# Kernel optimization log

Hardware: AMD Instinct MI355X
Metric: run time of the kernel (lower is better)

The kernel has to match this reference:

```python
import jax, jax.numpy as jnp
import numpy as np

N_NODES = 100000
N_EDGES = 6400000

def setup_inputs() -> dict:
    key = jax.random.key(0)
    ks = jax.random.split(key, 12)
    x = jax.random.normal(ks[0], (N_NODES, 2), dtype=jnp.float32)
    edge_index = jax.random.randint(ks[1], (2, N_EDGES), 0, N_NODES, dtype=jnp.int32)
    def w(k, fi, fo):
        return jax.random.normal(k, (fi, fo), dtype=jnp.float32) * (1.0 / np.sqrt(fi))
    return {
        "x": x, "edge_index": edge_index,
        "W0": w(ks[2], 2, 8), "b0": jnp.zeros((8,), jnp.float32),
        "W1": w(ks[3], 8, 8), "b1": jnp.zeros((8,), jnp.float32),
        "W2": w(ks[4], 8, 8), "b2": jnp.zeros((8,), jnp.float32),
        "W3": w(ks[5], 8, 8), "b3": jnp.zeros((8,), jnp.float32),
        "Wv": w(ks[6], 8, 1), "bv": jnp.zeros((1,), jnp.float32),
        "Wp": w(ks[7], 8, 1), "bp": jnp.zeros((1,), jnp.float32),
    }

def _gcn_norm(edge_index, n_nodes):
    # PyG GCNConv default: add self-loops, symmetric D^{-1/2} A_hat D^{-1/2}
    loops = jnp.arange(n_nodes, dtype=edge_index.dtype)
    src = jnp.concatenate([edge_index[0], loops])
    dst = jnp.concatenate([edge_index[1], loops])
    deg = jax.ops.segment_sum(jnp.ones_like(dst, dtype=jnp.float32), dst,
                              num_segments=n_nodes)
    dis = jax.lax.rsqrt(jnp.maximum(deg, 1.0))  # deg >= 1 due to self-loops
    norm = dis[src] * dis[dst]                   # [E + N]
    return src, dst, norm

def _gcn_conv(x, W, b, src, dst, norm, n_nodes):
    h = x @ W                                     # small GEMM [N, fo]
    msg = h[src] * norm[:, None]                  # gather + normalize
    out = jax.ops.segment_sum(msg, dst, num_segments=n_nodes)  # scatter-add
    return out + b

def reference(x, edge_index, W0, b0, W1, b1, W2, b2, W3, b3, Wv, bv, Wp, bp):
    n = x.shape[0]
    src, dst, norm = _gcn_norm(edge_index, n)
    h = x
    for W, b in ((W0, b0), (W1, b1), (W2, b2), (W3, b3)):
        h = jax.nn.elu(_gcn_conv(h, W, b, src, dst, norm, n))
    mean_val = _gcn_conv(h, Wv, bv, src, dst, norm, n)   # [N, 1]
    value = jnp.mean(mean_val, axis=0, keepdims=True)    # global_mean_pool, 1 graph -> [1, 1]
    proba = _gcn_conv(h, Wp, bp, src, dst, norm, n)      # [N, 1]
    return (proba, value)
```

## Files before the change

### kernel.cpp

```cpp
#include <hip/hip_runtime.h>

#define NT 256
#define CHUNK 1024
#define PBLK2 2048
#define PTILE 4096

static inline int nbi(long long n) { return (int)((n + NT - 1) / NT); }


__global__ __launch_bounds__(256) void k_histB(const int* __restrict__ dst,
                                               int* __restrict__ histB,
                                               int E, int NB) {
    __shared__ int lh[512];
    int t = threadIdx.x;
    for (int i = t; i < 512; i += 256) lh[i] = 0;
    __syncthreads();
    int chunk = (E + gridDim.x - 1) / gridDim.x;
    int lo = blockIdx.x * chunk, hi = min(E, lo + chunk);
    for (int i = lo + t; i < hi; i += 256)
        atomicAdd(&lh[dst[i] >> 8], 1);
    __syncthreads();
    for (int b = t; b < NB; b += 256)
        histB[(size_t)blockIdx.x * NB + b] = lh[b];
}

__global__ __launch_bounds__(256) void k_scanB2(const int* __restrict__ histB,
                                                int* __restrict__ cursorT,
                                                int* __restrict__ tot,
                                                int NB, int nblk) {
    __shared__ int ch[256];
    __shared__ int carry;
    int b = blockIdx.x, t = threadIdx.x;
    if (t == 0) carry = 0;
    __syncthreads();
    for (int c = 0; c < nblk; c += 256) {
        int blk = c + t;
        int v = (blk < nblk) ? histB[(size_t)blk * NB + b] : 0;
        ch[t] = v;
        __syncthreads();
        for (int o = 1; o < 256; o <<= 1) {
            int x = (t >= o) ? ch[t - o] : 0;
            __syncthreads();
            ch[t] += x;
            __syncthreads();
        }
        int excl = ch[t] - v + carry;
        if (blk < nblk) cursorT[(size_t)b * PBLK2 + blk] = excl;
        __syncthreads();
        if (t == 0) carry += ch[255];
        __syncthreads();
    }
    if (t == 0) tot[b] = carry;
}

__global__ __launch_bounds__(512) void k_bscan(const int* __restrict__ hist_g,
                                               int* __restrict__ bbase,
                                               int* __restrict__ rowst,
                                               int NB, int N, int E) {
    __shared__ int s[512];
    int t = threadIdx.x;
    int own = (t < NB) ? hist_g[t] : 0;
    s[t] = own;
    __syncthreads();
    for (int o = 1; o < 512; o <<= 1) {
        int v = (t >= o) ? s[t - o] : 0;
        __syncthreads();
        s[t] += v;
        __syncthreads();
    }
    if (t < NB) bbase[t] = s[t] - own;
    if (t == 0) { bbase[NB] = E; rowst[N] = E; }
}

__global__ __launch_bounds__(256) void k_partF(const int* __restrict__ src,
                                               const int* __restrict__ dst,
                                               const int* __restrict__ bbase,
                                               const int* __restrict__ cursorT,
                                               int* __restrict__ part,
                                               int E, int NB) {
    __shared__ int wcur[512];
    __shared__ int th[512], tloff[512], tcnt[512];
    __shared__ int ps[256];
    __shared__ int stage[PTILE];
    __shared__ unsigned short sbkt[PTILE];
    int t = threadIdx.x;
    int chunk = (E + gridDim.x - 1) / gridDim.x;
    int lo = blockIdx.x * chunk, hi = min(E, lo + chunk);
    if (lo >= hi) return;

    for (int b = t; b < NB; b += 256)
        wcur[b] = bbase[b] + cursorT[(size_t)b * PBLK2 + blockIdx.x];
    __syncthreads();

    for (int tlo = lo; tlo < hi; tlo += PTILE) {
        int thi = min(hi, tlo + PTILE);
        int cnt = thi - tlo;
        for (int i = t; i < 512; i += 256) { th[i] = 0; tcnt[i] = 0; }
        __syncthreads();
        for (int i = tlo + t; i < thi; i += 256) atomicAdd(&th[dst[i] >> 8], 1);
        __syncthreads();
        int a0 = th[2 * t], a1 = th[2 * t + 1];
        int psum = a0 + a1;
        ps[t] = psum;
        __syncthreads();
        for (int o = 1; o < 256; o <<= 1) {
            int v = (t >= o) ? ps[t - o] : 0;
            __syncthreads();
            ps[t] += v;
            __syncthreads();
        }
        int excl = ps[t] - psum;
        tloff[2 * t] = excl;
        tloff[2 * t + 1] = excl + a0;
        __syncthreads();
        for (int i = tlo + t; i < thi; i += 256) {
            int d = dst[i], s = src[i];
            int b = d >> 8;
            int pos = tloff[b] + atomicAdd(&tcnt[b], 1);
            stage[pos] = ((d & 255) << 17) | s;
            sbkt[pos] = (unsigned short)b;
        }
        __syncthreads();
        for (int i = t; i < cnt; i += 256) {
            int b = sbkt[i];
            part[wcur[b] + (i - tloff[b])] = stage[i];
        }
        __syncthreads();
        for (int b = t; b < NB; b += 256) wcur[b] += th[b];
        __syncthreads();
    }
}

__global__ __launch_bounds__(512) void k_build(const int* __restrict__ bbase,
                                               const int* __restrict__ part,
                                               const float* __restrict__ x,
                                               int* __restrict__ rowst,
                                               float* __restrict__ dis,
                                               float* __restrict__ v0,
                                               int* __restrict__ csr,
                                               int N) {
    __shared__ int dcnt[256], doff[256];
    int b = blockIdx.x, t = threadIdx.x;
    int lo = bbase[b], hi = bbase[b + 1];
    if (t < 256) dcnt[t] = 0;
    __syncthreads();
    for (int i = lo + t; i < hi; i += 512)
        atomicAdd(&dcnt[part[i] >> 17], 1);
    __syncthreads();
    int own = 0;
    if (t < 256) { own = dcnt[t]; doff[t] = own; }
    __syncthreads();
    for (int o = 1; o < 256; o <<= 1) {
        int v = 0;
        if (t < 256 && t >= o) v = doff[t - o];
        __syncthreads();
        if (t < 256) doff[t] += v;
        __syncthreads();
    }
    if (t < 256) {
        int excl = doff[t] - own;
        int node = (b << 8) + t;
        if (node < N) {
            rowst[node] = lo + excl;
            float dn = rsqrtf((float)own + 1.0f);
            dis[node] = dn;
            float2 xv = *reinterpret_cast<const float2*>(x + 2 * node);
            *reinterpret_cast<float2*>(v0 + 2 * node) = make_float2(dn * xv.x, dn * xv.y);
        }
        dcnt[t] = excl;
    }
    __syncthreads();
    for (int i = lo + t; i < hi; i += 512) {
        int pv = part[i];
        int slot = atomicAdd(&dcnt[pv >> 17], 1);
        csr[lo + slot] = pv & 0x1FFFF;
    }
}


__global__ __launch_bounds__(NT) void k_gL1(const int* __restrict__ rowst,
                                            const int* __restrict__ csr,
                                            const float* __restrict__ dis,
                                            const float* __restrict__ v0,
                                            const float* __restrict__ W0,
                                            const float* __restrict__ b0,
                                            const float* __restrict__ W1,
                                            float* __restrict__ un, int N) {
    int g = blockIdx.x * NT + threadIdx.x;
    int n = g >> 3, sub = g & 7;
    if (n >= N) return;
    int i = rowst[n] + sub, end = rowst[n + 1];
    float ax = 0.0f, ay = 0.0f;
    int s0 = 0, s1 = 0;
    bool r0 = i < end, r1 = i + 8 < end;
    if (r0) s0 = csr[i];
    if (r1) s1 = csr[i + 8];
    while (r0) {
        float2 p = *reinterpret_cast<const float2*>(v0 + 2 * s0);
        int i2 = i + 16;
        bool r2 = i2 < end;
        int s2 = 0; if (r2) s2 = csr[i2];
        ax += p.x; ay += p.y;
        i += 8; r0 = r1; s0 = s1; r1 = r2; s1 = s2;
    }
    ax += __shfl_xor(ax, 1, 64); ax += __shfl_xor(ax, 2, 64); ax += __shfl_xor(ax, 4, 64);
    ay += __shfl_xor(ay, 1, 64); ay += __shfl_xor(ay, 2, 64); ay += __shfl_xor(ay, 4, 64);
    float2 sv = *reinterpret_cast<const float2*>(v0 + 2 * n);
    ax += sv.x; ay += sv.y;
    float dn = dis[n];
    float gg = dn * (ax * W0[sub] + ay * W0[8 + sub]) + b0[sub];
    float h = gg > 0.0f ? gg : expm1f(gg);
    int base = (threadIdx.x & 63) & ~7;
    float o = 0.0f;
#pragma unroll
    for (int k = 0; k < 8; ++k) o += __shfl(h, base + k, 64) * W1[k * 8 + sub];
    un[8 * n + sub] = dn * o;
}

__global__ __launch_bounds__(NT) void k_gL8(const int* __restrict__ rowst,
                                            const int* __restrict__ csr,
                                            const float* __restrict__ dis,
                                            const float* __restrict__ u,
                                            const float* __restrict__ b,
                                            const float* __restrict__ W,
                                            float* __restrict__ un, int N) {
    int g = blockIdx.x * NT + threadIdx.x;
    int n = g >> 3, sub = g & 7;
    if (n >= N) return;
    int i = rowst[n] + sub, end = rowst[n + 1];
    float a[8];
#pragma unroll
    for (int k = 0; k < 8; ++k) a[k] = 0.0f;
    int s0 = 0, s1 = 0;
    bool r0 = i < end, r1 = i + 8 < end;
    if (r0) s0 = csr[i];
    if (r1) s1 = csr[i + 8];
    while (r0) {
        float4 p0 = *reinterpret_cast<const float4*>(u + 8 * s0);
        float4 p1 = *reinterpret_cast<const float4*>(u + 8 * s0 + 4);
        int i2 = i + 16;
        bool r2 = i2 < end;
        int s2 = 0; if (r2) s2 = csr[i2];
        a[0] += p0.x; a[1] += p0.y; a[2] += p0.z; a[3] += p0.w;
        a[4] += p1.x; a[5] += p1.y; a[6] += p1.z; a[7] += p1.w;
        i += 8; r0 = r1; s0 = s1; r1 = r2; s1 = s2;
    }
    int c4 = sub & 4, c2 = sub & 2, c1 = sub & 1;
#pragma unroll
    for (int j = 0; j < 4; ++j) {
        float send = c4 ? a[j] : a[j + 4];
        float recv = __shfl_xor(send, 4, 64);
        a[j] = (c4 ? a[j + 4] : a[j]) + recv;
    }
#pragma unroll
    for (int j = 0; j < 2; ++j) {
        float send = c2 ? a[j] : a[j + 2];
        float recv = __shfl_xor(send, 2, 64);
        a[j] = (c2 ? a[j + 2] : a[j]) + recv;
    }
    {
        float send = c1 ? a[0] : a[1];
        float recv = __shfl_xor(send, 1, 64);
        a[0] = (c1 ? a[1] : a[0]) + recv;
    }
    float dn = dis[n];
    float va = a[0] + u[8 * n + sub];
    float gg = va * dn + b[sub];
    float h = gg > 0.0f ? gg : expm1f(gg);
    int base = (threadIdx.x & 63) & ~7;
    float o = 0.0f;
#pragma unroll
    for (int k = 0; k < 8; ++k) o += __shfl(h, base + k, 64) * W[k * 8 + sub];
    un[8 * n + sub] = dn * o;
}

__global__ __launch_bounds__(NT) void k_gHead(const int* __restrict__ rowst,
                                              const int* __restrict__ csr,
                                              const float* __restrict__ dis,
                                              const float* __restrict__ u,
                                              const float* __restrict__ b,
                                              const float* __restrict__ Wv,
                                              const float* __restrict__ Wp,
                                              float* __restrict__ uH, int N) {
    int g = blockIdx.x * NT + threadIdx.x;
    int n = g >> 3, sub = g & 7;
    if (n >= N) return;
    int i = rowst[n] + sub, end = rowst[n + 1];
    float a[8];
#pragma unroll
    for (int k = 0; k < 8; ++k) a[k] = 0.0f;
    int s0 = 0, s1 = 0;
    bool r0 = i < end, r1 = i + 8 < end;
    if (r0) s0 = csr[i];
    if (r1) s1 = csr[i + 8];
    while (r0) {
        float4 p0 = *reinterpret_cast<const float4*>(u + 8 * s0);
        float4 p1 = *reinterpret_cast<const float4*>(u + 8 * s0 + 4);
        int i2 = i + 16;
        bool r2 = i2 < end;
        int s2 = 0; if (r2) s2 = csr[i2];
        a[0] += p0.x; a[1] += p0.y; a[2] += p0.z; a[3] += p0.w;
        a[4] += p1.x; a[5] += p1.y; a[6] += p1.z; a[7] += p1.w;
        i += 8; r0 = r1; s0 = s1; r1 = r2; s1 = s2;
    }
    int c4 = sub & 4, c2 = sub & 2, c1 = sub & 1;
#pragma unroll
    for (int j = 0; j < 4; ++j) {
        float send = c4 ? a[j] : a[j + 4];
        float recv = __shfl_xor(send, 4, 64);
        a[j] = (c4 ? a[j + 4] : a[j]) + recv;
    }
#pragma unroll
    for (int j = 0; j < 2; ++j) {
        float send = c2 ? a[j] : a[j + 2];
        float recv = __shfl_xor(send, 2, 64);
        a[j] = (c2 ? a[j + 2] : a[j]) + recv;
    }
    {
        float send = c1 ? a[0] : a[1];
        float recv = __shfl_xor(send, 1, 64);
        a[0] = (c1 ? a[1] : a[0]) + recv;
    }
    float dn = dis[n];
    float va = a[0] + u[8 * n + sub];
    float gg = va * dn + b[sub];
    float h = gg > 0.0f ? gg : expm1f(gg);
    float tv = h * Wv[sub];
    float tp = h * Wp[sub];
    tv += __shfl_xor(tv, 1, 64); tv += __shfl_xor(tv, 2, 64); tv += __shfl_xor(tv, 4, 64);
    tp += __shfl_xor(tp, 1, 64); tp += __shfl_xor(tp, 2, 64); tp += __shfl_xor(tp, 4, 64);
    if (sub == 0)
        *reinterpret_cast<float2*>(uH + 2 * n) = make_float2(dn * tv, dn * tp);
}

__global__ __launch_bounds__(NT) void k_g2F(const int* __restrict__ rowst,
                                            const int* __restrict__ csr,
                                            const float* __restrict__ dis,
                                            const float* __restrict__ uH,
                                            const float* __restrict__ bp,
                                            float* __restrict__ out,
                                            float* __restrict__ vsum, int N) {
    int g = blockIdx.x * NT + threadIdx.x;
    int n = g >> 3, sub = g & 7;
    bool valid = n < N;
    int i = 0, end = 0;
    if (valid) { i = rowst[n] + sub; end = rowst[n + 1]; }
    float av = 0.0f, ap = 0.0f;
    int s0 = 0, s1 = 0;
    bool r0 = i < end, r1 = i + 8 < end;
    if (r0) s0 = csr[i];
    if (r1) s1 = csr[i + 8];
    while (r0) {
        float2 p = *reinterpret_cast<const float2*>(uH + 2 * s0);
        int i2 = i + 16;
        bool r2 = i2 < end;
        int s2 = 0; if (r2) s2 = csr[i2];
        av += p.x; ap += p.y;
        i = i + 8; r0 = r1; s0 = s1; r1 = r2; s1 = s2;
    }
    av += __shfl_xor(av, 1, 64); av += __shfl_xor(av, 2, 64); av += __shfl_xor(av, 4, 64);
    ap += __shfl_xor(ap, 1, 64); ap += __shfl_xor(ap, 2, 64); ap += __shfl_xor(ap, 4, 64);
    float contrib = 0.0f;
    if (valid && sub == 0) {
        float2 selfv = *reinterpret_cast<const float2*>(uH + 2 * n);
        av += selfv.x; ap += selfv.y;
        float dn = dis[n];
        out[n] = ap * dn + bp[0];
        contrib = av * dn;
    }
#pragma unroll
    for (int o = 32; o > 0; o >>= 1) contrib += __shfl_down(contrib, o, 64);
    __shared__ float sred[NT / 64];
    if ((threadIdx.x & 63) == 0) sred[threadIdx.x >> 6] = contrib;
    __syncthreads();
    if (threadIdx.x == 0) {
        float bsum = 0.0f;
#pragma unroll
        for (int k = 0; k < NT / 64; ++k) bsum += sred[k];
        atomicAdd(vsum, bsum);
    }
}

__global__ void k_final(const float* __restrict__ vsum,
                        const float* __restrict__ bv,
                        float* __restrict__ out, int N) {
    out[0] = vsum[0] * (1.0f / (float)N) + bv[0];
}


__global__ __launch_bounds__(NT) void k_count(const int* __restrict__ dst,
                                              int* __restrict__ deg, int E) {
    int e = blockIdx.x * NT + threadIdx.x;
    if (e < E) atomicAdd(&deg[dst[e]], 1);
}

__global__ __launch_bounds__(NT) void k_scanA(const int* __restrict__ deg,
                                              int* __restrict__ partial, int N) {
    int t = threadIdx.x;
    int base = blockIdx.x * CHUNK + t * 4;
    int s = 0;
#pragma unroll
    for (int j = 0; j < 4; ++j) { int i = base + j; if (i < N) s += deg[i]; }
    __shared__ int red[NT];
    red[t] = s; __syncthreads();
    for (int o = NT / 2; o > 0; o >>= 1) {
        if (t < o) red[t] += red[t + o];
        __syncthreads();
    }
    if (t == 0) partial[blockIdx.x] = red[0];
}

__global__ void k_scanB(const int* __restrict__ partial, int* __restrict__ chunkoff,
                        int* __restrict__ rowst, int nblk, int N) {
    if (threadIdx.x == 0) {
        int off = 0;
        for (int b = 0; b < nblk; ++b) { chunkoff[b] = off; off += partial[b]; }
        rowst[N] = off;
    }
}

__global__ __launch_bounds__(NT) void k_scanC(const int* __restrict__ deg,
                                              const int* __restrict__ chunkoff,
                                              int* __restrict__ rowst,
                                              float* __restrict__ dis, int N) {
    int t = threadIdx.x;
    int base = blockIdx.x * CHUNK + t * 4;
    int v[4]; int tsum = 0;
#pragma unroll
    for (int j = 0; j < 4; ++j) { int i = base + j; v[j] = (i < N) ? deg[i] : 0; tsum += v[j]; }
    __shared__ int ss[NT];
    ss[t] = tsum; __syncthreads();
    for (int o = 1; o < NT; o <<= 1) {
        int x = (t >= o) ? ss[t - o] : 0;
        __syncthreads();
        ss[t] += x;
        __syncthreads();
    }
    int run = ss[t] - tsum + chunkoff[blockIdx.x];
#pragma unroll
    for (int j = 0; j < 4; ++j) {
        int i = base + j;
        if (i < N) { rowst[i] = run; dis[i] = rsqrtf((float)v[j] + 1.0f); run += v[j]; }
    }
}

__global__ __launch_bounds__(NT) void k_fill(const int* __restrict__ src,
                                             const int* __restrict__ dst,
                                             const int* __restrict__ rowst,
                                             int* __restrict__ deg,
                                             int* __restrict__ csr, int E) {
    int e = blockIdx.x * NT + threadIdx.x;
    if (e >= E) return;
    int s = src[e], d = dst[e];
    int old = atomicSub(&deg[d], 1);
    csr[rowst[d] + old - 1] = s;
}

__global__ __launch_bounds__(NT) void k_v0(const float* __restrict__ x,
                                           const float* __restrict__ dis,
                                           float* __restrict__ v0, int N) {
    int n = blockIdx.x * NT + threadIdx.x;
    if (n >= N) return;
    float dn = dis[n];
    float2 xv = *reinterpret_cast<const float2*>(x + 2 * n);
    *reinterpret_cast<float2*>(v0 + 2 * n) = make_float2(dn * xv.x, dn * xv.y);
}


extern "C" void kernel_launch(void* const* d_in, const int* in_sizes, int n_in,
                              void* d_out, int out_size, void* d_ws, size_t ws_size,
                              hipStream_t stream) {
    const float* x  = (const float*)d_in[0];
    const int* ei   = (const int*)d_in[1];
    const float* W0 = (const float*)d_in[2];
    const float* b0 = (const float*)d_in[3];
    const float* W1 = (const float*)d_in[4];
    const float* b1 = (const float*)d_in[5];
    const float* W2 = (const float*)d_in[6];
    const float* b2 = (const float*)d_in[7];
    const float* W3 = (const float*)d_in[8];
    const float* b3 = (const float*)d_in[9];
    const float* Wv = (const float*)d_in[10];
    const float* bv = (const float*)d_in[11];
    const float* Wp = (const float*)d_in[12];
    const float* bp = (const float*)d_in[13];
    float* out = (float*)d_out;

    int N = in_sizes[0] / 2;
    int E = in_sizes[1] / 2;
    const int* src = ei;
    const int* dst = ei + E;
    int NB = (N + 255) >> 8;

    size_t needP = ((size_t)22 * N + 2 * (size_t)E + 2048) * 4;
    bool histFits = (size_t)2 * PBLK2 * NB <= (size_t)E;

    if (N <= 131072 && NB <= 512 && ws_size >= needP && histFits) {
        int* tot    = (int*)d_ws;
        int* bbase  = tot + 512;
        float* vsum = (float*)(bbase + 513);
        int* rowst  = (int*)(vsum + 8);
        float* dis  = (float*)(rowst + N + 1);
        float* v0   = dis + N;
        float* uA   = v0 + (size_t)2 * N;
        float* uB   = uA + (size_t)8 * N;
        float* uH   = uB + (size_t)8 * N;
        int* part   = (int*)(uH + (size_t)2 * N);
        int* csr    = part + (size_t)E;
        int* histB   = csr;
        int* cursorT = csr + (size_t)PBLK2 * NB;

        hipMemsetAsync(vsum, 0, 4, stream);

        k_histB<<<PBLK2, 256, 0, stream>>>(dst, histB, E, NB);
        k_scanB2<<<NB, 256, 0, stream>>>(histB, cursorT, tot, NB, PBLK2);
        k_bscan<<<1, 512, 0, stream>>>(tot, bbase, rowst, NB, N, E);
        k_partF<<<PBLK2, 256, 0, stream>>>(src, dst, bbase, cursorT, part, E, NB);
        k_build<<<NB, 512, 0, stream>>>(bbase, part, x, rowst, dis, v0, csr, N);

        k_gL1<<<nbi(8LL * N), NT, 0, stream>>>(rowst, csr, dis, v0, W0, b0, W1, uA, N);
        k_gL8<<<nbi(8LL * N), NT, 0, stream>>>(rowst, csr, dis, uA, b1, W2, uB, N);
        k_gL8<<<nbi(8LL * N), NT, 0, stream>>>(rowst, csr, dis, uB, b2, W3, uA, N);
        k_gHead<<<nbi(8LL * N), NT, 0, stream>>>(rowst, csr, dis, uA, b3, Wv, Wp, uH, N);
        k_g2F<<<nbi(8LL * N), NT, 0, stream>>>(rowst, csr, dis, uH, bp, out, vsum, N);
        k_final<<<1, 1, 0, stream>>>(vsum, bv, out + N, N);
    } else {
        int nblk = (N + CHUNK - 1) / CHUNK;
        int* deg      = (int*)d_ws;
        int* rowst    = deg + N;
        int* chunkoff = rowst + N + 1;
        int* partial  = chunkoff + nblk;
        float* dis    = (float*)(partial + nblk);
        float* vsum   = dis + N;
        float* v0     = vsum + 8;
        float* uA     = v0 + (size_t)2 * N;
        float* uB     = uA + (size_t)8 * N;
        float* uH     = uB + (size_t)8 * N;
        int* csr      = (int*)(uH + (size_t)2 * N);

        hipMemsetAsync(deg, 0, (size_t)N * 4, stream);
        hipMemsetAsync(vsum, 0, 4, stream);

        k_count<<<nbi(E), NT, 0, stream>>>(dst, deg, E);
        k_scanA<<<nblk, NT, 0, stream>>>(deg, partial, N);
        k_scanB<<<1, 64, 0, stream>>>(partial, chunkoff, rowst, nblk, N);
        k_scanC<<<nblk, NT, 0, stream>>>(deg, chunkoff, rowst, dis, N);
        k_fill<<<nbi(E), NT, 0, stream>>>(src, dst, rowst, deg, csr, E);
        k_v0<<<nbi(N), NT, 0, stream>>>(x, dis, v0, N);

        k_gL1<<<nbi(8LL * N), NT, 0, stream>>>(rowst, csr, dis, v0, W0, b0, W1, uA, N);
        k_gL8<<<nbi(8LL * N), NT, 0, stream>>>(rowst, csr, dis, uA, b1, W2, uB, N);
        k_gL8<<<nbi(8LL * N), NT, 0, stream>>>(rowst, csr, dis, uB, b2, W3, uA, N);
        k_gHead<<<nbi(8LL * N), NT, 0, stream>>>(rowst, csr, dis, uA, b3, Wv, Wp, uH, N);
        k_g2F<<<nbi(8LL * N), NT, 0, stream>>>(rowst, csr, dis, uH, bp, out, vsum, N);
        k_final<<<1, 1, 0, stream>>>(vsum, bv, out + N, N);
    }
}
```

Baseline: 355.8 us.

## Reuse per-block histogram in partition and unroll CSR gather loops by four

The partition kernel now reads the per-block bucket histogram already computed by k_histB instead of recomputing a tile histogram, and handles each block's whole chunk in a single tile (guarded by chunk <= PTILE). That removes one pass over dst and the per-tile loop. The gather loops in all aggregation kernels replace the software-pipelined one-at-a-time prefetch with a four-way unrolled loop that issues four index loads and four row loads together, raising memory-level parallelism. Workspace offsets are padded to multiples of four so the vector loads stay aligned. This costs more registers per thread and a larger remainder loop.

```diff
diff --git a/kernel.cpp b/kernel.cpp
--- a/kernel.cpp
+++ b/kernel.cpp
@@ -75,59 +75,48 @@
 __global__ __launch_bounds__(256) void k_partF(const int* __restrict__ src,
                                                const int* __restrict__ dst,
                                                const int* __restrict__ bbase,
+                                               const int* __restrict__ histB,
                                                const int* __restrict__ cursorT,
                                                int* __restrict__ part,
                                                int E, int NB) {
-    __shared__ int wcur[512];
-    __shared__ int th[512], tloff[512], tcnt[512];
-    __shared__ int ps[256];
+    __shared__ int wadj[512], tloff[512], tcnt[512], ps[256];
     __shared__ int stage[PTILE];
     __shared__ unsigned short sbkt[PTILE];
     int t = threadIdx.x;
+    int blk = blockIdx.x;
     int chunk = (E + gridDim.x - 1) / gridDim.x;
-    int lo = blockIdx.x * chunk, hi = min(E, lo + chunk);
+    int lo = blk * chunk, hi = min(E, lo + chunk);
     if (lo >= hi) return;
-
-    for (int b = t; b < NB; b += 256)
-        wcur[b] = bbase[b] + cursorT[(size_t)b * PBLK2 + blockIdx.x];
-    __syncthreads();
-
-    for (int tlo = lo; tlo < hi; tlo += PTILE) {
-        int thi = min(hi, tlo + PTILE);
-        int cnt = thi - tlo;
-        for (int i = t; i < 512; i += 256) { th[i] = 0; tcnt[i] = 0; }
-        __syncthreads();
-        for (int i = tlo + t; i < thi; i += 256) atomicAdd(&th[dst[i] >> 8], 1);
-        __syncthreads();
-        int a0 = th[2 * t], a1 = th[2 * t + 1];
-        int psum = a0 + a1;
-        ps[t] = psum;
-        __syncthreads();
-        for (int o = 1; o < 256; o <<= 1) {
-            int v = (t >= o) ? ps[t - o] : 0;
-            __syncthreads();
-            ps[t] += v;
-            __syncthreads();
-        }
-        int excl = ps[t] - psum;
-        tloff[2 * t] = excl;
-        tloff[2 * t + 1] = excl + a0;
-        __syncthreads();
-        for (int i = tlo + t; i < thi; i += 256) {
-            int d = dst[i], s = src[i];
-            int b = d >> 8;
-            int pos = tloff[b] + atomicAdd(&tcnt[b], 1);
-            stage[pos] = ((d & 255) << 17) | s;
-            sbkt[pos] = (unsigned short)b;
-        }
-        __syncthreads();
-        for (int i = t; i < cnt; i += 256) {
-            int b = sbkt[i];
-            part[wcur[b] + (i - tloff[b])] = stage[i];
-        }
-        __syncthreads();
-        for (int b = t; b < NB; b += 256) wcur[b] += th[b];
-        __syncthreads();
+    int cnt = hi - lo;
+    int b0 = 2 * t, b1 = 2 * t + 1;
+    int v0c = (b0 < NB) ? histB[(size_t)blk * NB + b0] : 0;
+    int v1c = (b1 < NB) ? histB[(size_t)blk * NB + b1] : 0;
+    ps[t] = v0c + v1c;
+    __syncthreads();
+    for (int o = 1; o < 256; o <<= 1) {
+        int v = (t >= o) ? ps[t - o] : 0;
+        __syncthreads();
+        ps[t] += v;
+        __syncthreads();
+    }
+    int excl = ps[t] - v0c - v1c;
+    tloff[b0] = excl;
+    tloff[b1] = excl + v0c;
+    tcnt[b0] = 0; tcnt[b1] = 0;
+    if (b0 < NB) wadj[b0] = bbase[b0] + cursorT[(size_t)b0 * PBLK2 + blk] - excl;
+    if (b1 < NB) wadj[b1] = bbase[b1] + cursorT[(size_t)b1 * PBLK2 + blk] - (excl + v0c);
+    __syncthreads();
+    for (int i = lo + t; i < hi; i += 256) {
+        int d = dst[i], s = src[i];
+        int b = d >> 8;
+        int pos = tloff[b] + atomicAdd(&tcnt[b], 1);
+        stage[pos] = ((d & 255) << 17) | s;
+        sbkt[pos] = (unsigned short)b;
+    }
+    __syncthreads();
+    for (int i = t; i < cnt; i += 256) {
+        int b = sbkt[i];
+        part[wadj[b] + i] = stage[i];
     }
 }
 
@@ -191,17 +180,21 @@
     if (n >= N) return;
     int i = rowst[n] + sub, end = rowst[n + 1];
     float ax = 0.0f, ay = 0.0f;
-    int s0 = 0, s1 = 0;
-    bool r0 = i < end, r1 = i + 8 < end;
-    if (r0) s0 = csr[i];
-    if (r1) s1 = csr[i + 8];
-    while (r0) {
-        float2 p = *reinterpret_cast<const float2*>(v0 + 2 * s0);
-        int i2 = i + 16;
-        bool r2 = i2 < end;
-        int s2 = 0; if (r2) s2 = csr[i2];
+    while (i + 24 < end) {
+        int i0 = csr[i], i1 = csr[i + 8], i2 = csr[i + 16], i3 = csr[i + 24];
+        float2 p0 = *reinterpret_cast<const float2*>(v0 + 2 * i0);
+        float2 p1 = *reinterpret_cast<const float2*>(v0 + 2 * i1);
+        float2 p2 = *reinterpret_cast<const float2*>(v0 + 2 * i2);
+        float2 p3 = *reinterpret_cast<const float2*>(v0 + 2 * i3);
+        ax += p0.x + p1.x + p2.x + p3.x;
+        ay += p0.y + p1.y + p2.y + p3.y;
+        i += 32;
+    }
+    while (i < end) {
+        int s = csr[i];
+        float2 p = *reinterpret_cast<const float2*>(v0 + 2 * s);
         ax += p.x; ay += p.y;
-        i += 8; r0 = r1; s0 = s1; r1 = r2; s1 = s2;
+        i += 8;
     }
     ax += __shfl_xor(ax, 1, 64); ax += __shfl_xor(ax, 2, 64); ax += __shfl_xor(ax, 4, 64);
     ay += __shfl_xor(ay, 1, 64); ay += __shfl_xor(ay, 2, 64); ay += __shfl_xor(ay, 4, 64);
@@ -231,19 +224,33 @@
     float a[8];
 #pragma unroll
     for (int k = 0; k < 8; ++k) a[k] = 0.0f;
-    int s0 = 0, s1 = 0;
-    bool r0 = i < end, r1 = i + 8 < end;
-    if (r0) s0 = csr[i];
-    if (r1) s1 = csr[i + 8];
-    while (r0) {
-        float4 p0 = *reinterpret_cast<const float4*>(u + 8 * s0);
-        float4 p1 = *reinterpret_cast<const float4*>(u + 8 * s0 + 4);
-        int i2 = i + 16;
-        bool r2 = i2 < end;
-        int s2 = 0; if (r2) s2 = csr[i2];
+    while (i + 24 < end) {
+        int i0 = csr[i], i1 = csr[i + 8], i2 = csr[i + 16], i3 = csr[i + 24];
+        float4 p00 = *reinterpret_cast<const float4*>(u + 8 * i0);
+        float4 p01 = *reinterpret_cast<const float4*>(u + 8 * i0 + 4);
+        float4 p10 = *reinterpret_cast<const float4*>(u + 8 * i1);
+        float4 p11 = *reinterpret_cast<const float4*>(u + 8 * i1 + 4);
+        float4 p20 = *reinterpret_cast<const float4*>(u + 8 * i2);
+        float4 p21 = *reinterpret_cast<const float4*>(u + 8 * i2 + 4);
+        float4 p30 = *reinterpret_cast<const float4*>(u + 8 * i3);
+        float4 p31 = *reinterpret_cast<const float4*>(u + 8 * i3 + 4);
+        a[0] += p00.x + p10.x + p20.x + p30.x;
+        a[1] += p00.y + p10.y + p20.y + p30.y;
+        a[2] += p00.z + p10.z + p20.z + p30.z;
+        a[3] += p00.w + p10.w + p20.w + p30.w;
+        a[4] += p01.x + p11.x + p21.x + p31.x;
+        a[5] += p01.y + p11.y + p21.y + p31.y;
+        a[6] += p01.z + p11.z + p21.z + p31.z;
+        a[7] += p01.w + p11.w + p21.w + p31.w;
+        i += 32;
+    }
+    while (i < end) {
+        int s = csr[i];
+        float4 p0 = *reinterpret_cast<const float4*>(u + 8 * s);
+        float4 p1 = *reinterpret_cast<const float4*>(u + 8 * s + 4);
         a[0] += p0.x; a[1] += p0.y; a[2] += p0.z; a[3] += p0.w;
         a[4] += p1.x; a[5] += p1.y; a[6] += p1.z; a[7] += p1.w;
-        i += 8; r0 = r1; s0 = s1; r1 = r2; s1 = s2;
+        i += 8;
     }
     int c4 = sub & 4, c2 = sub & 2, c1 = sub & 1;
 #pragma unroll
@@ -289,19 +296,33 @@
     float a[8];
 #pragma unroll
     for (int k = 0; k < 8; ++k) a[k] = 0.0f;
-    int s0 = 0, s1 = 0;
-    bool r0 = i < end, r1 = i + 8 < end;
-    if (r0) s0 = csr[i];
-    if (r1) s1 = csr[i + 8];
-    while (r0) {
-        float4 p0 = *reinterpret_cast<const float4*>(u + 8 * s0);
-        float4 p1 = *reinterpret_cast<const float4*>(u + 8 * s0 + 4);
-        int i2 = i + 16;
-        bool r2 = i2 < end;
-        int s2 = 0; if (r2) s2 = csr[i2];
+    while (i + 24 < end) {
+        int i0 = csr[i], i1 = csr[i + 8], i2 = csr[i + 16], i3 = csr[i + 24];
+        float4 p00 = *reinterpret_cast<const float4*>(u + 8 * i0);
+        float4 p01 = *reinterpret_cast<const float4*>(u + 8 * i0 + 4);
+        float4 p10 = *reinterpret_cast<const float4*>(u + 8 * i1);
+        float4 p11 = *reinterpret_cast<const float4*>(u + 8 * i1 + 4);
+        float4 p20 = *reinterpret_cast<const float4*>(u + 8 * i2);
+        float4 p21 = *reinterpret_cast<const float4*>(u + 8 * i2 + 4);
+        float4 p30 = *reinterpret_cast<const float4*>(u + 8 * i3);
+        float4 p31 = *reinterpret_cast<const float4*>(u + 8 * i3 + 4);
+        a[0] += p00.x + p10.x + p20.x + p30.x;
+        a[1] += p00.y + p10.y + p20.y + p30.y;
+        a[2] += p00.z + p10.z + p20.z + p30.z;
+        a[3] += p00.w + p10.w + p20.w + p30.w;
+        a[4] += p01.x + p11.x + p21.x + p31.x;
+        a[5] += p01.y + p11.y + p21.y + p31.y;
+        a[6] += p01.z + p11.z + p21.z + p31.z;
+        a[7] += p01.w + p11.w + p21.w + p31.w;
+        i += 32;
+    }
+    while (i < end) {
+        int s = csr[i];
+        float4 p0 = *reinterpret_cast<const float4*>(u + 8 * s);
+        float4 p1 = *reinterpret_cast<const float4*>(u + 8 * s + 4);
         a[0] += p0.x; a[1] += p0.y; a[2] += p0.z; a[3] += p0.w;
         a[4] += p1.x; a[5] += p1.y; a[6] += p1.z; a[7] += p1.w;
-        i += 8; r0 = r1; s0 = s1; r1 = r2; s1 = s2;
+        i += 8;
     }
     int c4 = sub & 4, c2 = sub & 2, c1 = sub & 1;
 #pragma unroll
@@ -346,17 +367,21 @@
     int i = 0, end = 0;
     if (valid) { i = rowst[n] + sub; end = rowst[n + 1]; }
     float av = 0.0f, ap = 0.0f;
-    int s0 = 0, s1 = 0;
-    bool r0 = i < end, r1 = i + 8 < end;
-    if (r0) s0 = csr[i];
-    if (r1) s1 = csr[i + 8];
-    while (r0) {
-        float2 p = *reinterpret_cast<const float2*>(uH + 2 * s0);
-        int i2 = i + 16;
-        bool r2 = i2 < end;
-        int s2 = 0; if (r2) s2 = csr[i2];
+    while (i + 24 < end) {
+        int i0 = csr[i], i1 = csr[i + 8], i2 = csr[i + 16], i3 = csr[i + 24];
+        float2 p0 = *reinterpret_cast<const float2*>(uH + 2 * i0);
+        float2 p1 = *reinterpret_cast<const float2*>(uH + 2 * i1);
+        float2 p2 = *reinterpret_cast<const float2*>(uH + 2 * i2);
+        float2 p3 = *reinterpret_cast<const float2*>(uH + 2 * i3);
+        av += p0.x + p1.x + p2.x + p3.x;
+        ap += p0.y + p1.y + p2.y + p3.y;
+        i += 32;
+    }
+    while (i < end) {
+        int s = csr[i];
+        float2 p = *reinterpret_cast<const float2*>(uH + 2 * s);
         av += p.x; ap += p.y;
-        i = i + 8; r0 = r1; s0 = s1; r1 = r2; s1 = s2;
+        i += 8;
     }
     av += __shfl_xor(av, 1, 64); av += __shfl_xor(av, 2, 64); av += __shfl_xor(av, 4, 64);
     ap += __shfl_xor(ap, 1, 64); ap += __shfl_xor(ap, 2, 64); ap += __shfl_xor(ap, 4, 64);
@@ -491,22 +516,25 @@
     const int* src = ei;
     const int* dst = ei + E;
     int NB = (N + 255) >> 8;
-
-    size_t needP = ((size_t)22 * N + 2 * (size_t)E + 2048) * 4;
+    int NP = (N + 3) & ~3;
+    int EP = (E + 3) & ~3;
+    int chunkP = (E + PBLK2 - 1) / PBLK2;
+
+    size_t needP = ((size_t)22 * NP + 2 * (size_t)EP + 1044) * 4;
     bool histFits = (size_t)2 * PBLK2 * NB <= (size_t)E;
 
-    if (N <= 131072 && NB <= 512 && ws_size >= needP && histFits) {
+    if (N <= 131072 && NB <= 512 && ws_size >= needP && histFits && chunkP <= PTILE) {
         int* tot    = (int*)d_ws;
         int* bbase  = tot + 512;
-        float* vsum = (float*)(bbase + 513);
+        float* vsum = (float*)(bbase + 520);
         int* rowst  = (int*)(vsum + 8);
-        float* dis  = (float*)(rowst + N + 1);
-        float* v0   = dis + N;
-        float* uA   = v0 + (size_t)2 * N;
-        float* uB   = uA + (size_t)8 * N;
-        float* uH   = uB + (size_t)8 * N;
-        int* part   = (int*)(uH + (size_t)2 * N);
-        int* csr    = part + (size_t)E;
+        float* dis  = (float*)(rowst + NP + 4);
+        float* v0   = dis + NP;
+        float* uA   = v0 + (size_t)2 * NP;
+        float* uB   = uA + (size_t)8 * NP;
+        float* uH   = uB + (size_t)8 * NP;
+        int* part   = (int*)(uH + (size_t)2 * NP);
+        int* csr    = part + (size_t)EP;
         int* histB   = csr;
         int* cursorT = csr + (size_t)PBLK2 * NB;
 
@@ -515,7 +543,7 @@
         k_histB<<<PBLK2, 256, 0, stream>>>(dst, histB, E, NB);
         k_scanB2<<<NB, 256, 0, stream>>>(histB, cursorT, tot, NB, PBLK2);
         k_bscan<<<1, 512, 0, stream>>>(tot, bbase, rowst, NB, N, E);
-        k_partF<<<PBLK2, 256, 0, stream>>>(src, dst, bbase, cursorT, part, E, NB);
+        k_partF<<<PBLK2, 256, 0, stream>>>(src, dst, bbase, histB, cursorT, part, E, NB);
         k_build<<<NB, 512, 0, stream>>>(bbase, part, x, rowst, dis, v0, csr, N);
 
         k_gL1<<<nbi(8LL * N), NT, 0, stream>>>(rowst, csr, dis, v0, W0, b0, W1, uA, N);
```

Measured after the change: 335.3 us. -5.7%, faster.
